# Kernel optimization log

Hardware: AMD Instinct MI355X
Metric: run time of the kernel (lower is better)

Reference implementation:

```python
import jax, jax.numpy as jnp
import numpy as np

HID = 3584
NH = 28
NKV = 4
HD = HID // NH  # 128
T = 2048
THETA = 1000000.0
SCALE = HD ** -0.5


def setup_inputs() -> dict:
    key = jax.random.key(0)
    ks = jax.random.split(key, 9)
    s = 0.02
    return {
        "positions": jnp.arange(T, dtype=jnp.int32),
        "hidden_states": jax.random.normal(ks[0], (T, HID), dtype=jnp.float32),
        "wq": jax.random.normal(ks[1], (HID, NH * HD), dtype=jnp.float32) * s,
        "bq": jax.random.normal(ks[2], (NH * HD,), dtype=jnp.float32) * s,
        "wk": jax.random.normal(ks[3], (HID, NKV * HD), dtype=jnp.float32) * s,
        "bk": jax.random.normal(ks[4], (NKV * HD,), dtype=jnp.float32) * s,
        "wv": jax.random.normal(ks[5], (HID, NKV * HD), dtype=jnp.float32) * s,
        "bv": jax.random.normal(ks[6], (NKV * HD,), dtype=jnp.float32) * s,
        "wo": jax.random.normal(ks[7], (NH * HD, HID), dtype=jnp.float32) * s,
    }


def _rope(x, positions):
    # neox-style RoPE over full head_dim: split halves, rotate.
    half = HD // 2
    inv_freq = 1.0 / (THETA ** (jnp.arange(0, half, dtype=jnp.float32) / half))
    ang = positions.astype(jnp.float32)[:, None] * inv_freq  # [T, half]
    cos = jnp.cos(ang)[:, None, :]  # [T, 1, half]
    sin = jnp.sin(ang)[:, None, :]
    x1, x2 = x[..., :half], x[..., half:]
    return jnp.concatenate([x1 * cos - x2 * sin, x2 * cos + x1 * sin], axis=-1)


def reference(positions, hidden_states, wq, bq, wk, bk, wv, bv, wo):
    q = (hidden_states @ wq + bq).reshape(T, NH, HD)
    k = (hidden_states @ wk + bk).reshape(T, NKV, HD)
    v = (hidden_states @ wv + bv).reshape(T, NKV, HD)
    q = _rope(q, positions)
    k = _rope(k, positions)
    # GQA: expand kv heads to query heads (groups of NH//NKV)
    g = NH // NKV
    k = jnp.repeat(k, g, axis=1)  # [T, NH, HD]
    v = jnp.repeat(v, g, axis=1)
    scores = jnp.einsum("thd,shd->hts", q, k) * SCALE  # bidirectional, no mask
    probs = jax.nn.softmax(scores, axis=-1)
    attn = jnp.einsum("hts,shd->thd", probs, v).reshape(T, NH * HD)
    return attn @ wo
```

## Files before the change

### kernel.cpp

```cpp
#include <hip/hip_runtime.h>

typedef __bf16 bf16_t;
typedef __attribute__((ext_vector_type(8))) __bf16 bf16x8;
typedef __attribute__((ext_vector_type(4))) float floatx4;

#define T_SEQ 2048
#define HID 3584
#define NH 28
#define NKV 4
#define HD 128
#define GQA 7
#define SCALE_F 0.08838834764831845f
#define QSCALE_LOG2 0.1275179100693744f

__global__ void conv_bf_k(const float* __restrict__ src, bf16_t* __restrict__ dst, long n) {
  const long i = ((long)blockIdx.x * 256 + threadIdx.x) * 8;
  if (i >= n) return;
  const floatx4 a = *(const floatx4*)(src + i);
  const floatx4 b = *(const floatx4*)(src + i + 4);
  bf16x8 r;
  r[0] = (bf16_t)a[0]; r[1] = (bf16_t)a[1]; r[2] = (bf16_t)a[2]; r[3] = (bf16_t)a[3];
  r[4] = (bf16_t)b[0]; r[5] = (bf16_t)b[1]; r[6] = (bf16_t)b[2]; r[7] = (bf16_t)b[3];
  *(bf16x8*)(dst + i) = r;
}

__global__ void bias_cat_k(const float* __restrict__ bq, const float* __restrict__ bk,
                           const float* __restrict__ bv, float* __restrict__ dst) {
  const int i = blockIdx.x * 256 + threadIdx.x;
  if (i < 3584) dst[i] = bq[i];
  else if (i < 4096) dst[i] = bk[i - 3584];
  else if (i < 4608) dst[i] = bv[i - 4096];
}

__global__ __launch_bounds__(256) void tconv_k(const float* __restrict__ src,
                                               bf16_t* __restrict__ dst, long N, long K) {
  __shared__ alignas(16) bf16_t t[64][72];
  const long k0 = (long)blockIdx.y * 64, n0 = (long)blockIdx.x * 64;
  const int tid = threadIdx.x;
  const int rr = tid >> 4;
  const int cc = (tid & 15) * 4;
#pragma unroll
  for (int i = 0; i < 4; ++i) {
    const int r = rr + i * 16;
    const floatx4 v = *(const floatx4*)(src + (k0 + r) * N + n0 + cc);
#pragma unroll
    for (int j = 0; j < 4; ++j) t[cc + j][r] = (bf16_t)v[j];
  }
  __syncthreads();
#pragma unroll
  for (int i = 0; i < 2; ++i) {
    const int J = i * 256 + tid;
    const int n = J >> 3, c8 = (J & 7) * 8;
    *(bf16x8*)(dst + (n0 + n) * K + k0 + c8) = *(const bf16x8*)(&t[n][c8]);
  }
}

__global__ __launch_bounds__(256) void tconv_kv_k(const float* __restrict__ wk,
                                                  const float* __restrict__ wv,
                                                  bf16_t* __restrict__ dst, long K) {
  __shared__ alignas(16) bf16_t t[64][72];
  const int bx = blockIdx.x;
  const float* src = (bx < 8) ? wk : wv;
  const long n0s = (long)(bx & 7) * 64;
  const long n0d = (long)bx * 64;
  const long k0 = (long)blockIdx.y * 64;
  const int tid = threadIdx.x;
  const int rr = tid >> 4;
  const int cc = (tid & 15) * 4;
#pragma unroll
  for (int i = 0; i < 4; ++i) {
    const int r = rr + i * 16;
    const floatx4 v = *(const floatx4*)(src + (k0 + r) * 512 + n0s + cc);
#pragma unroll
    for (int j = 0; j < 4; ++j) t[cc + j][r] = (bf16_t)v[j];
  }
  __syncthreads();
#pragma unroll
  for (int i = 0; i < 2; ++i) {
    const int J = i * 256 + tid;
    const int n = J >> 3, c8 = (J & 7) * 8;
    *(bf16x8*)(dst + (n0d + n) * K + k0 + c8) = *(const bf16x8*)(&t[n][c8]);
  }
}

__device__ __forceinline__ bf16x8 ld8(const void* p, long idx, bool f32) {
  if (f32) {
    const float* q = (const float*)p + idx;
    const floatx4 u = *(const floatx4*)q;
    const floatx4 v = *(const floatx4*)(q + 4);
    bf16x8 r;
    r[0] = (bf16_t)u[0]; r[1] = (bf16_t)u[1]; r[2] = (bf16_t)u[2]; r[3] = (bf16_t)u[3];
    r[4] = (bf16_t)v[0]; r[5] = (bf16_t)v[1]; r[6] = (bf16_t)v[2]; r[7] = (bf16_t)v[3];
    return r;
  }
  return *(const bf16x8*)((const bf16_t*)p + idx);
}

__device__ __forceinline__ void gld16(const bf16_t* g, bf16_t* l) {
  __builtin_amdgcn_global_load_lds(
      (const __attribute__((address_space(1))) unsigned int*)(const void*)g,
      (__attribute__((address_space(3))) unsigned int*)(void*)l, 16, 0, 0);
}

__global__ __launch_bounds__(256) void gemm_bt_k(
    const bf16_t* __restrict__ A, long lda,
    const bf16_t* __restrict__ Bt, long ldb,
    const float* __restrict__ bias, void* Cv, long ldc,
    int K, int mode, void* Cv2) {
  __shared__ alignas(16) bf16_t ldsA[2][128 * 32];
  __shared__ alignas(16) bf16_t ldsB[2][128 * 32];
  const int tid = threadIdx.x;
  const int lane = tid & 63;
  const int w = tid >> 6;
  const int wr = w >> 1, wc = w & 1;
  const int col = lane & 15, quad = lane >> 4;
  const long m0 = (long)blockIdx.y * 128, n0 = (long)blockIdx.x * 128;

  const int r0 = tid >> 2;
  const int c0 = tid & 3;
  const int cs = c0 ^ ((r0 >> 1) & 3);
  const int r1 = 64 + r0;

  const bf16_t* Ab = A + m0 * lda + cs * 8;
  const bf16_t* Bb = Bt + n0 * ldb + cs * 8;

  floatx4 acc[4][4] = {};
  const int nt = K >> 5;

  auto stage = [&](int buf, int t) {
    const long k0 = (long)t << 5;
    gld16(Ab + (long)r0 * lda + k0, ldsA[buf] + tid * 8);
    gld16(Ab + (long)r1 * lda + k0, ldsA[buf] + (256 + tid) * 8);
    gld16(Bb + (long)r0 * ldb + k0, ldsB[buf] + tid * 8);
    gld16(Bb + (long)r1 * ldb + k0, ldsB[buf] + (256 + tid) * 8);
  };

  stage(0, 0);
  for (int t = 0; t < nt; ++t) {
    const int cur = t & 1;
    stage(cur ^ 1, (t + 1 == nt) ? 0 : t + 1);
    __builtin_amdgcn_sched_barrier(0);
    asm volatile("s_waitcnt vmcnt(4)" ::: "memory");
    __builtin_amdgcn_sched_barrier(0);
    __builtin_amdgcn_s_barrier();
    __builtin_amdgcn_sched_barrier(0);
    bf16x8 af[4], bf[4];
#pragma unroll
    for (int i = 0; i < 4; ++i) {
      const int ra = wr * 64 + i * 16 + col;
      af[i] = *(const bf16x8*)(ldsA[cur] + ra * 32 + (quad ^ ((ra >> 1) & 3)) * 8);
    }
#pragma unroll
    for (int j = 0; j < 4; ++j) {
      const int rb = wc * 64 + j * 16 + col;
      bf[j] = *(const bf16x8*)(ldsB[cur] + rb * 32 + (quad ^ ((rb >> 1) & 3)) * 8);
    }
#pragma unroll
    for (int i = 0; i < 4; ++i)
#pragma unroll
      for (int j = 0; j < 4; ++j)
        acc[i][j] = __builtin_amdgcn_mfma_f32_16x16x32_bf16(af[i], bf[j], acc[i][j], 0, 0, 0);
    __builtin_amdgcn_sched_barrier(0);
    __builtin_amdgcn_s_barrier();
    __builtin_amdgcn_sched_barrier(0);
  }

#pragma unroll
  for (int i = 0; i < 4; ++i) {
#pragma unroll
    for (int j = 0; j < 4; ++j) {
      const long row0 = m0 + wr * 64 + i * 16 + quad * 4;
      const long cc = n0 + wc * 64 + j * 16 + col;
      const float bvv = bias ? bias[cc] : 0.f;
#pragma unroll
      for (int r = 0; r < 4; ++r) {
        const float v = acc[i][j][r] + bvv;
        if (mode == 0)      ((bf16_t*)Cv)[(row0 + r) * ldc + cc] = (bf16_t)v;
        else if (mode == 1) ((float*)Cv)[(row0 + r) * ldc + cc] = v;
        else {
          if (cc < 3584)      ((bf16_t*)Cv)[(row0 + r) * ldc + cc] = (bf16_t)v;
          else if (cc < 4096) ((bf16_t*)Cv2)[(row0 + r) * 512 + (cc - 3584)] = (bf16_t)v;
          else ((bf16_t*)Cv2)[1048576 + (cc - 4096) * (long)T_SEQ + (row0 + r)] = (bf16_t)v;
        }
      }
    }
  }
}

__global__ __launch_bounds__(256) void gemm_nt_k(
    const void* A, long lda, const void* B, long ldb,
    const float* bias, void* Cv, long ldc,
    int K, int aMode, int bMode, int transC, int c32, const int* flag) {
  __shared__ alignas(16) bf16_t ldsA[128 * 32];
  __shared__ alignas(16) unsigned int ldsB32[128 * 16];
  const int f = *flag;
  const bool aF32 = aMode && (f > 32);
  const bool bF32 = bMode && (f > 32);
  const int tid = threadIdx.x;
  const int lane = tid & 63;
  const int w = tid >> 6;
  const int wr = w >> 1, wc = w & 1;
  const int col = lane & 15, quad = lane >> 4;
  const long m0 = (long)blockIdx.y * 128, n0 = (long)blockIdx.x * 128;

  const int ar1 = tid >> 2, ak = (tid & 3) * 8;
  const int ar2 = 64 + ar1;
  const int kk = (tid >> 4) * 2;
  const int nn = (tid & 15) * 8;
  const int kp = kk >> 1;

  floatx4 acc[4][4] = {};

  for (int k0 = 0; k0 < K; k0 += 32) {
    const bf16x8 a1 = ld8(A, (m0 + ar1) * lda + k0 + ak, aF32);
    const bf16x8 a2 = ld8(A, (m0 + ar2) * lda + k0 + ak, aF32);
    const bf16x8 b0 = ld8(B, (long)(k0 + kk) * ldb + n0 + nn, bF32);
    const bf16x8 b1 = ld8(B, (long)(k0 + kk + 1) * ldb + n0 + nn, bF32);
    __syncthreads();
    *(bf16x8*)(ldsA + ar1 * 32 + ak) = a1;
    *(bf16x8*)(ldsA + ar2 * 32 + ak) = a2;
#pragma unroll
    for (int j = 0; j < 8; ++j) {
      const int n = nn + j;
      const int pk = ((((kp >> 2) ^ ((n >> 3) & 3)) << 2) | (kp & 3));
      union { struct { bf16_t lo, hi; } s; unsigned int u; } cv;
      cv.s.lo = b0[j];
      cv.s.hi = b1[j];
      ldsB32[n * 16 + pk] = cv.u;
    }
    __syncthreads();
    bf16x8 af[4], bfv[4];
#pragma unroll
    for (int i = 0; i < 4; ++i)
      af[i] = *(const bf16x8*)(ldsA + (wr * 64 + i * 16 + col) * 32 + quad * 8);
#pragma unroll
    for (int j = 0; j < 4; ++j) {
      const int n = wc * 64 + j * 16 + col;
      const int blk = quad ^ ((n >> 3) & 3);
      bfv[j] = *(const bf16x8*)((const bf16_t*)(ldsB32 + n * 16 + blk * 4));
    }
#pragma unroll
    for (int i = 0; i < 4; ++i)
#pragma unroll
      for (int jj = 0; jj < 4; ++jj)
        acc[i][jj] = __builtin_amdgcn_mfma_f32_16x16x32_bf16(af[i], bfv[jj], acc[i][jj], 0, 0, 0);
  }

#pragma unroll
  for (int i = 0; i < 4; ++i) {
#pragma unroll
    for (int j = 0; j < 4; ++j) {
      const long row0 = m0 + wr * 64 + i * 16 + quad * 4;
      const long cc = n0 + wc * 64 + j * 16 + col;
      const float bvv = bias ? bias[cc] : 0.f;
#pragma unroll
      for (int r = 0; r < 4; ++r) {
        const float v = acc[i][j][r] + bvv;
        if (transC)   ((bf16_t*)Cv)[cc * ldc + (row0 + r)] = (bf16_t)v;
        else if (c32) ((float*)Cv)[(row0 + r) * ldc + cc] = v;
        else          ((bf16_t*)Cv)[(row0 + r) * ldc + cc] = (bf16_t)v;
      }
    }
  }
}

__global__ void rope2_k(bf16_t* __restrict__ qb, bf16_t* __restrict__ kb,
                        const int* __restrict__ pos) {
  const int idx = blockIdx.x * 256 + threadIdx.x;
  const int qtot = T_SEQ * NH * 64;
  bf16_t* buf;
  long ld;
  int nheads, id;
  if (idx < qtot) { buf = qb; ld = HID; nheads = NH; id = idx; }
  else { buf = kb; ld = 512; nheads = NKV; id = idx - qtot; }
  const int d = id & 63;
  const int th = id >> 6;
  const int h = th % nheads;
  const int t = th / nheads;
  const float inv = exp2f((float)d * (-19.931568569324174f / 64.f));
  const float ang = (float)pos[t] * inv;
  float sn, cs;
  __sincosf(ang, &sn, &cs);
  bf16_t* p = buf + (long)t * ld + h * HD + d;
  const float x1 = (float)p[0];
  const float x2 = (float)p[64];
  p[0] = (bf16_t)(x1 * cs - x2 * sn);
  p[64] = (bf16_t)(x2 * cs + x1 * sn);
}

__global__ void rope_k(bf16_t* buf, const int* __restrict__ pos, long ld, int nheads) {
  const int idx = blockIdx.x * 256 + threadIdx.x;
  const int total = T_SEQ * nheads * 64;
  if (idx >= total) return;
  const int d = idx & 63;
  const int th = idx >> 6;
  const int h = th % nheads;
  const int t = th / nheads;
  const float inv = exp2f((float)d * (-19.931568569324174f / 64.f));
  const float ang = (float)pos[t] * inv;
  float sn, cs;
  __sincosf(ang, &sn, &cs);
  bf16_t* p = buf + (long)t * ld + h * HD + d;
  const float x1 = (float)p[0];
  const float x2 = (float)p[64];
  p[0] = (bf16_t)(x1 * cs - x2 * sn);
  p[64] = (bf16_t)(x2 * cs + x1 * sn);
}

__global__ __launch_bounds__(256, 2) void attn5_k(
    const bf16_t* __restrict__ q, long qs,
    const bf16_t* __restrict__ k, long ks,
    const bf16_t* __restrict__ vt,
    bf16_t* __restrict__ out, long os) {
  __shared__ alignas(16) bf16_t ldsK[2][64 * 128];
  __shared__ alignas(16) bf16_t ldsV[2][128 * 64];
  __shared__ alignas(16) bf16_t pbuf[4][32 * 64];

  const int h = blockIdx.y;
  const long hkvHD = (long)(h / GQA) * HD;
  const int tid = threadIdx.x;
  const int lane = tid & 63;
  const int w = tid >> 6;
  const int col = lane & 15, quad = lane >> 4;
  const int t0 = blockIdx.x * 128 + w * 32;

  auto stage = [&](int buf, int t) {
    const long s0 = (long)t * 64;
#pragma unroll
    for (int i = 0; i < 4; ++i) {
      const int J = i * 256 + tid;
      {
        const int row = J >> 4;
        const int cs = (J & 15) ^ (row & 7);
        gld16(k + (s0 + row) * ks + hkvHD + cs * 8, &ldsK[buf][J * 8]);
      }
      {
        const int row = J >> 3;
        const int cs = (J & 7) ^ (row & 7);
        gld16(vt + (hkvHD + row) * T_SEQ + s0 + cs * 8, &ldsV[buf][J * 8]);
      }
    }
  };

  bf16x8 aq[2][4];
#pragma unroll
  for (int sub = 0; sub < 2; ++sub) {
    const bf16_t* qp = q + (long)(t0 + sub * 16 + col) * qs + h * HD + quad * 8;
#pragma unroll
    for (int c = 0; c < 4; ++c) {
      aq[sub][c] = *(const bf16x8*)(qp + c * 32);
#pragma unroll
      for (int e = 0; e < 8; ++e)
        aq[sub][c][e] = (bf16_t)((float)aq[sub][c][e] * QSCALE_LOG2);
    }
  }

  bf16x8 ones;
#pragma unroll
  for (int e = 0; e < 8; ++e) ones[e] = (bf16_t)1.0f;

  floatx4 O[2][8] = {};
  float m_w[2] = {-1e30f, -1e30f};
  float l_i[2][4] = {};

  stage(0, 0);
  for (int t = 0; t < 32; ++t) {
    const int cur = t & 1;
    stage(cur ^ 1, (t + 1) & 31);
    __builtin_amdgcn_sched_barrier(0);
    asm volatile("s_waitcnt vmcnt(8)" ::: "memory");
    __builtin_amdgcn_sched_barrier(0);
    __builtin_amdgcn_s_barrier();
    __builtin_amdgcn_sched_barrier(0);

    floatx4 S[2][4] = {};
    __builtin_amdgcn_s_setprio(1);
#pragma unroll
    for (int nt = 0; nt < 4; ++nt) {
      const int row = nt * 16 + col;
#pragma unroll
      for (int c = 0; c < 4; ++c) {
        const int cs = (c * 4 + quad) ^ (row & 7);
        const bf16x8 bk = *(const bf16x8*)(&ldsK[cur][row * 128 + cs * 8]);
        S[0][nt] = __builtin_amdgcn_mfma_f32_16x16x32_bf16(aq[0][c], bk, S[0][nt], 0, 0, 0);
        S[1][nt] = __builtin_amdgcn_mfma_f32_16x16x32_bf16(aq[1][c], bk, S[1][nt], 0, 0, 0);
      }
    }
    __builtin_amdgcn_s_setprio(0);

#pragma unroll
    for (int sub = 0; sub < 2; ++sub) {
      float mx = S[sub][0][0];
#pragma unroll
      for (int nt = 0; nt < 4; ++nt)
#pragma unroll
        for (int r = 0; r < 4; ++r) mx = fmaxf(mx, S[sub][nt][r]);
#pragma unroll
      for (int off = 1; off < 64; off <<= 1)
        mx = fmaxf(mx, __shfl_xor(mx, off, 64));
      if (mx > m_w[sub] + 12.0f) {
        const float alpha = exp2f(m_w[sub] - mx);
        m_w[sub] = mx;
#pragma unroll
        for (int r = 0; r < 4; ++r) l_i[sub][r] *= alpha;
#pragma unroll
        for (int dt = 0; dt < 8; ++dt)
#pragma unroll
          for (int r = 0; r < 4; ++r) O[sub][dt][r] *= alpha;
      }
    }

#pragma unroll
    for (int sub = 0; sub < 2; ++sub)
#pragma unroll
      for (int r = 0; r < 4; ++r) {
        const int mrow = sub * 16 + quad * 4 + r;
#pragma unroll
        for (int nt = 0; nt < 4; ++nt) {
          const float p = exp2f(S[sub][nt][r] - m_w[sub]);
          const int cs = (nt * 2 + (col >> 3)) ^ (mrow & 7);
          pbuf[w][mrow * 64 + cs * 8 + (col & 7)] = (bf16_t)p;
        }
      }

    floatx4 Ssum[2] = {};
    __builtin_amdgcn_s_setprio(1);
#pragma unroll
    for (int kb = 0; kb < 2; ++kb) {
      const int csp = (kb * 4 + quad) ^ (col & 7);
      const bf16x8 pa0 = *(const bf16x8*)(&pbuf[w][(col) * 64 + csp * 8]);
      const bf16x8 pa1 = *(const bf16x8*)(&pbuf[w][(16 + col) * 64 + csp * 8]);
      Ssum[0] = __builtin_amdgcn_mfma_f32_16x16x32_bf16(pa0, ones, Ssum[0], 0, 0, 0);
      Ssum[1] = __builtin_amdgcn_mfma_f32_16x16x32_bf16(pa1, ones, Ssum[1], 0, 0, 0);
#pragma unroll
      for (int dt = 0; dt < 8; ++dt) {
        const int vrow = dt * 16 + col;
        const bf16x8 bv = *(const bf16x8*)(&ldsV[cur][vrow * 64 + csp * 8]);
        O[0][dt] = __builtin_amdgcn_mfma_f32_16x16x32_bf16(pa0, bv, O[0][dt], 0, 0, 0);
        O[1][dt] = __builtin_amdgcn_mfma_f32_16x16x32_bf16(pa1, bv, O[1][dt], 0, 0, 0);
      }
    }
    __builtin_amdgcn_s_setprio(0);
#pragma unroll
    for (int sub = 0; sub < 2; ++sub)
#pragma unroll
      for (int r = 0; r < 4; ++r) l_i[sub][r] += Ssum[sub][r];

    __builtin_amdgcn_sched_barrier(0);
    __builtin_amdgcn_s_barrier();
    __builtin_amdgcn_sched_barrier(0);
  }

#pragma unroll
  for (int sub = 0; sub < 2; ++sub) {
#pragma unroll
    for (int r = 0; r < 4; ++r) l_i[sub][r] = 1.f / l_i[sub][r];
#pragma unroll
    for (int dt = 0; dt < 8; ++dt) {
#pragma unroll
      for (int r = 0; r < 4; ++r) {
        const long trow = t0 + sub * 16 + quad * 4 + r;
        out[trow * os + h * HD + dt * 16 + col] = (bf16_t)(O[sub][dt][r] * l_i[sub][r]);
      }
    }
  }
}

extern "C" void kernel_launch(void* const* d_in, const int* in_sizes, int n_in,
                              void* d_out_v, int out_size, void* d_ws, size_t ws_size,
                              hipStream_t stream) {
  const int* pos = (const int*)d_in[0];
  const float* hidden = (const float*)d_in[1];
  const float* wq = (const float*)d_in[2];
  const float* bq = (const float*)d_in[3];
  const float* wk = (const float*)d_in[4];
  const float* bk = (const float*)d_in[5];
  const float* wv = (const float*)d_in[6];
  const float* bv = (const float*)d_in[7];
  const float* wo = (const float*)d_in[8];

  bf16_t* qbuf = (bf16_t*)d_out_v;
  bf16_t* attn_hi = (bf16_t*)d_out_v + (size_t)T_SEQ * HID;
  float* outf = (float*)d_out_v;

  char* ws = (char*)d_ws;
  const size_t NEED = 51904516;

  if (ws_size >= NEED) {
    bf16_t* hbf  = (bf16_t*)ws;
    bf16_t* wqbt = (bf16_t*)(ws + 14680064);
    bf16_t* wkbt = (bf16_t*)(ws + 40370176);
    bf16_t* kbuf = (bf16_t*)(ws + 47710208);
    bf16_t* vt   = (bf16_t*)(ws + 49807360);
    bf16_t* wobt = wqbt;
    bf16_t* attnb = hbf;
    float* bqkv = (float*)attn_hi;

    bias_cat_k<<<18, 256, 0, stream>>>(bq, bk, bv, bqkv);
    conv_bf_k<<<3584, 256, 0, stream>>>(hidden, hbf, (long)T_SEQ * HID);
    tconv_k<<<dim3(56, 56), 256, 0, stream>>>(wq, wqbt, HID, HID);
    tconv_kv_k<<<dim3(16, 56), 256, 0, stream>>>(wk, wv, wkbt, HID);

    gemm_bt_k<<<dim3(36, 16), 256, 0, stream>>>(hbf, HID, wqbt, HID, bqkv, qbuf, HID,
                                                HID, 3, kbuf);

    rope2_k<<<(T_SEQ * (NH + NKV) * 64) / 256, 256, 0, stream>>>(qbuf, kbuf, pos);

    attn5_k<<<dim3(16, 28), 256, 0, stream>>>(qbuf, HID, kbuf, 512, vt, attnb, HID);

    tconv_k<<<dim3(56, 56), 256, 0, stream>>>(wo, wobt, HID, HID);

    gemm_bt_k<<<dim3(28, 16), 256, 0, stream>>>(attnb, HID, wobt, HID, nullptr,
                                                outf, HID, HID, 1, nullptr);
  } else {
    bf16_t* kbuf = (bf16_t*)ws;
    bf16_t* vt = (bf16_t*)(ws + 2097152);
    bf16_t* acopy = (bf16_t*)ws;
    int* flag = (int*)(ws + 4194304);

    hipMemsetAsync(flag, 64, 4, stream);

    gemm_nt_k<<<dim3(28, 16), 256, 0, stream>>>(hidden, HID, wq, HID, bq, qbuf, HID,
                                                HID, 1, 1, 0, 0, flag);
    gemm_nt_k<<<dim3(4, 16), 256, 0, stream>>>(hidden, HID, wk, 512, bk, kbuf, 512,
                                               HID, 1, 1, 0, 0, flag);
    gemm_nt_k<<<dim3(4, 16), 256, 0, stream>>>(hidden, HID, wv, 512, bv, vt, T_SEQ,
                                               HID, 1, 1, 1, 0, flag);

    rope_k<<<(T_SEQ * NH * 64) / 256, 256, 0, stream>>>(qbuf, pos, HID, NH);
    rope_k<<<(T_SEQ * NKV * 64) / 256, 256, 0, stream>>>(kbuf, pos, 512, NKV);

    attn5_k<<<dim3(16, 28), 256, 0, stream>>>(qbuf, HID, kbuf, 512, vt, attn_hi, HID);

    hipMemcpyAsync(acopy, attn_hi + (size_t)1536 * HID, (size_t)512 * HID * 2,
                   hipMemcpyDeviceToDevice, stream);
    gemm_nt_k<<<dim3(28, 8), 256, 0, stream>>>(attn_hi, HID, wo, HID, nullptr,
                                               outf, HID, HID, 0, 1, 0, 1, flag);
    gemm_nt_k<<<dim3(28, 4), 256, 0, stream>>>(attn_hi + (size_t)1024 * HID, HID, wo, HID,
                                               nullptr, outf + (size_t)1024 * HID, HID,
                                               HID, 0, 1, 0, 1, flag);
    gemm_nt_k<<<dim3(28, 4), 256, 0, stream>>>(acopy, HID, wo, HID,
                                               nullptr, outf + (size_t)1536 * HID, HID,
                                               HID, 0, 1, 0, 1, flag);
  }
}
```

Baseline: 492.1 us.

## Use persistent attention kernel with atomic work queue and 16-row waves

Measured after the change: 531.2 us. 1.08x slower.

```diff
diff --git a/kernel.cpp b/kernel.cpp
--- a/kernel.cpp
+++ b/kernel.cpp
@@ -307,6 +307,165 @@
   p[64] = (bf16_t)(x2 * cs + x1 * sn);
 }
 
+__global__ __launch_bounds__(256, 2) void attn6_k(
+    const bf16_t* __restrict__ q, long qs,
+    const bf16_t* __restrict__ k, long ks,
+    const bf16_t* __restrict__ vt,
+    bf16_t* __restrict__ out, long os,
+    int* __restrict__ counter) {
+  __shared__ alignas(16) bf16_t ldsK[2][64 * 128];
+  __shared__ alignas(16) bf16_t ldsV[2][128 * 64];
+  __shared__ alignas(16) bf16_t pbuf[4][16 * 64];
+  __shared__ int item_s;
+
+  const int tid = threadIdx.x;
+  const int lane = tid & 63;
+  const int w = tid >> 6;
+  const int col = lane & 15, quad = lane >> 4;
+
+  bf16x8 ones;
+#pragma unroll
+  for (int e = 0; e < 8; ++e) ones[e] = (bf16_t)1.0f;
+
+  while (true) {
+    __syncthreads();
+    if (tid == 0) item_s = atomicAdd(counter, 1);
+    __syncthreads();
+    const int item = item_s;
+    if (item >= NH * 32) break;
+
+    const int h = item >> 5;
+    const int qt = item & 31;
+    const long hkvHD = (long)(h / GQA) * HD;
+    const int t0 = qt * 64 + w * 16;
+
+    auto stage = [&](int buf, int t) {
+      const long s0 = (long)t * 64;
+#pragma unroll
+      for (int i = 0; i < 4; ++i) {
+        const int J = i * 256 + tid;
+        {
+          const int row = J >> 4;
+          const int cs = (J & 15) ^ (row & 7);
+          gld16(k + (s0 + row) * ks + hkvHD + cs * 8, &ldsK[buf][J * 8]);
+        }
+        {
+          const int row = J >> 3;
+          const int cs = (J & 7) ^ (row & 7);
+          gld16(vt + (hkvHD + row) * T_SEQ + s0 + cs * 8, &ldsV[buf][J * 8]);
+        }
+      }
+    };
+
+    bf16x8 aq[4];
+    {
+      const bf16_t* qp = q + (long)(t0 + col) * qs + h * HD + quad * 8;
+#pragma unroll
+      for (int c = 0; c < 4; ++c) {
+        aq[c] = *(const bf16x8*)(qp + c * 32);
+#pragma unroll
+        for (int e = 0; e < 8; ++e)
+          aq[c][e] = (bf16_t)((float)aq[c][e] * QSCALE_LOG2);
+      }
+    }
+
+    floatx4 O[8] = {};
+    float m_w = -1e30f;
+    floatx4 l_v = {};
+
+    stage(0, 0);
+    for (int t = 0; t < 32; ++t) {
+      const int cur = t & 1;
+      if (t < 31) {
+        stage(cur ^ 1, t + 1);
+        __builtin_amdgcn_sched_barrier(0);
+        asm volatile("s_waitcnt vmcnt(8)" ::: "memory");
+      } else {
+        __builtin_amdgcn_sched_barrier(0);
+        asm volatile("s_waitcnt vmcnt(0)" ::: "memory");
+      }
+      __builtin_amdgcn_sched_barrier(0);
+      __builtin_amdgcn_s_barrier();
+      __builtin_amdgcn_sched_barrier(0);
+
+      floatx4 S[4] = {};
+      __builtin_amdgcn_s_setprio(1);
+#pragma unroll
+      for (int nt = 0; nt < 4; ++nt) {
+        const int row = nt * 16 + col;
+#pragma unroll
+        for (int c = 0; c < 4; ++c) {
+          const int cs = (c * 4 + quad) ^ (row & 7);
+          const bf16x8 bk = *(const bf16x8*)(&ldsK[cur][row * 128 + cs * 8]);
+          S[nt] = __builtin_amdgcn_mfma_f32_16x16x32_bf16(aq[c], bk, S[nt], 0, 0, 0);
+        }
+      }
+      __builtin_amdgcn_s_setprio(0);
+
+      float mx = S[0][0];
+#pragma unroll
+      for (int nt = 0; nt < 4; ++nt)
+#pragma unroll
+        for (int r = 0; r < 4; ++r) mx = fmaxf(mx, S[nt][r]);
+#pragma unroll
+      for (int off = 1; off < 64; off <<= 1)
+        mx = fmaxf(mx, __shfl_xor(mx, off, 64));
+      if (mx > m_w + 12.0f) {
+        const float alpha = exp2f(m_w - mx);
+        m_w = mx;
+#pragma unroll
+        for (int r = 0; r < 4; ++r) l_v[r] *= alpha;
+#pragma unroll
+        for (int dt = 0; dt < 8; ++dt)
+#pragma unroll
+          for (int r = 0; r < 4; ++r) O[dt][r] *= alpha;
+      }
+
+#pragma unroll
+      for (int r = 0; r < 4; ++r) {
+        const int mrow = quad * 4 + r;
+#pragma unroll
+        for (int nt = 0; nt < 4; ++nt) {
+          const float p = exp2f(S[nt][r] - m_w);
+          const int cs = (nt * 2 + (col >> 3)) ^ (mrow & 7);
+          pbuf[w][mrow * 64 + cs * 8 + (col & 7)] = (bf16_t)p;
+        }
+      }
+
+      __builtin_amdgcn_s_setprio(1);
+#pragma unroll
+      for (int kb = 0; kb < 2; ++kb) {
+        const int csp = (kb * 4 + quad) ^ (col & 7);
+        const bf16x8 pa = *(const bf16x8*)(&pbuf[w][col * 64 + csp * 8]);
+        l_v = __builtin_amdgcn_mfma_f32_16x16x32_bf16(pa, ones, l_v, 0, 0, 0);
+#pragma unroll
+        for (int dt = 0; dt < 8; ++dt) {
+          const int vrow = dt * 16 + col;
+          const bf16x8 bv = *(const bf16x8*)(&ldsV[cur][vrow * 64 + csp * 8]);
+          O[dt] = __builtin_amdgcn_mfma_f32_16x16x32_bf16(pa, bv, O[dt], 0, 0, 0);
+        }
+      }
+      __builtin_amdgcn_s_setprio(0);
+
+      __builtin_amdgcn_sched_barrier(0);
+      __builtin_amdgcn_s_barrier();
+      __builtin_amdgcn_sched_barrier(0);
+    }
+
+    float li[4];
+#pragma unroll
+    for (int r = 0; r < 4; ++r) li[r] = 1.f / l_v[r];
+#pragma unroll
+    for (int dt = 0; dt < 8; ++dt) {
+#pragma unroll
+      for (int r = 0; r < 4; ++r) {
+        const long trow = t0 + quad * 4 + r;
+        out[trow * os + h * HD + dt * 16 + col] = (bf16_t)(O[dt][r] * li[r]);
+      }
+    }
+  }
+}
+
 __global__ __launch_bounds__(256, 2) void attn5_k(
     const bf16_t* __restrict__ q, long qs,
     const bf16_t* __restrict__ k, long ks,
@@ -492,10 +651,12 @@
     bf16_t* wkbt = (bf16_t*)(ws + 40370176);
     bf16_t* kbuf = (bf16_t*)(ws + 47710208);
     bf16_t* vt   = (bf16_t*)(ws + 49807360);
+    int* counter = (int*)(ws + 51904512);
     bf16_t* wobt = wqbt;
     bf16_t* attnb = hbf;
     float* bqkv = (float*)attn_hi;
 
+    hipMemsetAsync(counter, 0, 4, stream);
     bias_cat_k<<<18, 256, 0, stream>>>(bq, bk, bv, bqkv);
     conv_bf_k<<<3584, 256, 0, stream>>>(hidden, hbf, (long)T_SEQ * HID);
     tconv_k<<<dim3(56, 56), 256, 0, stream>>>(wq, wqbt, HID, HID);
@@ -506,7 +667,7 @@
 
     rope2_k<<<(T_SEQ * (NH + NKV) * 64) / 256, 256, 0, stream>>>(qbuf, kbuf, pos);
 
-    attn5_k<<<dim3(16, 28), 256, 0, stream>>>(qbuf, HID, kbuf, 512, vt, attnb, HID);
+    attn6_k<<<512, 256, 0, stream>>>(qbuf, HID, kbuf, 512, vt, attnb, HID, counter);
 
     tconv_k<<<dim3(56, 56), 256, 0, stream>>>(wo, wobt, HID, HID);
 
```
